# Optimization experiments

Hardware: AMD Instinct MI355X
Metric: run time of the kernel (lower is better)

Reference implementation:

```python
import jax, jax.numpy as jnp
import numpy as np

DIM = 4096
N_HEADS = 32
N_KV = 8
HEAD_DIM = DIM // N_HEADS  # 128
ROPE_THETA = 10000.0


def setup_inputs() -> dict:
    key = jax.random.key(0)
    ks = jax.random.split(key, 5)
    B, S = 1, 2048
    x = jax.random.normal(ks[0], (B, S, DIM), jnp.float32)
    wq = jax.random.normal(ks[1], (N_HEADS * HEAD_DIM, DIM), jnp.float32) * 0.02
    wk = jax.random.normal(ks[2], (N_KV * HEAD_DIM, DIM), jnp.float32) * 0.02
    wv = jax.random.normal(ks[3], (N_KV * HEAD_DIM, DIM), jnp.float32) * 0.02
    wo = jax.random.normal(ks[4], (DIM, DIM), jnp.float32) * 0.02
    # precomputed RoPE frequencies: angle[t, i] = t / theta^(2i/head_dim)
    inv_freq = 1.0 / (ROPE_THETA ** (jnp.arange(0, HEAD_DIM, 2, dtype=jnp.float32) / HEAD_DIM))
    t = jnp.arange(S, dtype=jnp.float32)
    angles = jnp.outer(t, inv_freq)  # [S, HEAD_DIM/2]
    return {"x": x, "wq": wq, "wk": wk, "wv": wv, "wo": wo,
            "freqs_cos": jnp.cos(angles), "freqs_sin": jnp.sin(angles)}


def _apply_rope(v, cos, sin):
    # v: [B, S, H, HEAD_DIM]; cos/sin: [S, HEAD_DIM/2]
    # mirrors torch view_as_complex on (..., hd/2, 2): even idx = real, odd idx = imag
    vr = v.reshape(*v.shape[:-1], HEAD_DIM // 2, 2)
    xr, xi = vr[..., 0], vr[..., 1]
    c = cos[None, :, None, :]
    s = sin[None, :, None, :]
    out_r = xr * c - xi * s
    out_i = xr * s + xi * c
    return jnp.stack([out_r, out_i], axis=-1).reshape(v.shape)


def reference(x, wq, wk, wv, wo, freqs_cos, freqs_sin):
    B, S, _ = x.shape
    rep = N_HEADS // N_KV
    q = (x @ wq.T).reshape(B, S, N_HEADS, HEAD_DIM)
    k = (x @ wk.T).reshape(B, S, N_KV, HEAD_DIM)
    v = (x @ wv.T).reshape(B, S, N_KV, HEAD_DIM)
    q = _apply_rope(q, freqs_cos, freqs_sin)
    k = _apply_rope(k, freqs_cos, freqs_sin)
    # native GQA: group query heads per kv head instead of materializing repeated KV
    qg = q.reshape(B, S, N_KV, rep, HEAD_DIM)
    scale = 1.0 / jnp.sqrt(jnp.asarray(HEAD_DIM, jnp.float32))
    scores = jnp.einsum('bqkrd,bskd->bkrqs', qg, k) * scale  # [B, n_kv, rep, S, S]
    causal = jnp.tril(jnp.ones((S, S), bool))
    scores = jnp.where(causal, scores, -jnp.inf)
    probs = jax.nn.softmax(scores, axis=-1)
    out = jnp.einsum('bkrqs,bskd->bqkrd', probs, v).reshape(B, S, DIM)
    return out @ wo.T
```

## Files before the change

kernel.cpp:

```cpp
#include <hip/hip_runtime.h>
#include <cstdint>

typedef __attribute__((ext_vector_type(8))) __bf16 bf16x8;
typedef __attribute__((ext_vector_type(4))) float  f32x4;
typedef __attribute__((ext_vector_type(8))) unsigned short ushort8;

#define DIM 4096
#define SEQ 2048
#define NH  32
#define NKV 8
#define HD  128

__device__ __forceinline__ float b2f(unsigned short u) {
  union { unsigned int i; float f; } v; v.i = ((unsigned int)u) << 16; return v.f;
}
__device__ __forceinline__ unsigned short f2b(float f) {
  union { float f; unsigned int i; } v; v.f = f;
  unsigned int r = v.i + 0x7fffu + ((v.i >> 16) & 1u);
  return (unsigned short)(r >> 16);
}

__device__ __forceinline__ void gl_lds16(const void* g, void* l) {
  __builtin_amdgcn_global_load_lds(
      (const __attribute__((address_space(1))) void*)(uintptr_t)g,
      (__attribute__((address_space(3))) void*)(uintptr_t)l,
      16, 0, 0);
}

__global__ __launch_bounds__(256) void f32_to_bf16(const float* __restrict__ src,
                                                   unsigned short* __restrict__ dst, int n) {
  const int i = (blockIdx.x * 256 + threadIdx.x) * 8;
  if (i >= n) return;
  const float4 a = *(const float4*)(src + i);
  const float4 b = *(const float4*)(src + i + 4);
  ushort8 o;
  o[0] = f2b(a.x); o[1] = f2b(a.y); o[2] = f2b(a.z); o[3] = f2b(a.w);
  o[4] = f2b(b.x); o[5] = f2b(b.y); o[6] = f2b(b.z); o[7] = f2b(b.w);
  *(ushort8*)(dst + i) = o;
}

template <bool OUT_F32>
__global__ __launch_bounds__(256) void gemm_bt(const unsigned short* __restrict__ A,
                                               const unsigned short* __restrict__ B,
                                               void* __restrict__ Cv,
                                               int M, int N, int K) {
  __shared__ __align__(16) unsigned short As[128 * 32];
  __shared__ __align__(16) unsigned short Bs[128 * 32];
  const int n0   = blockIdx.x * 128;
  const int m0   = blockIdx.y * 128;
  const int tid  = threadIdx.x;
  const int w    = tid >> 6;
  const int lane = tid & 63;
  const int quad = lane >> 4;
  const int l15  = lane & 15;
  const int wm   = (w & 1) * 64;
  const int wn   = (w >> 1) * 64;

  const f32x4 fzero = {0.f, 0.f, 0.f, 0.f};
  f32x4 acc[4][4];
#pragma unroll
  for (int i = 0; i < 4; ++i)
#pragma unroll
    for (int j = 0; j < 4; ++j) acc[i][j] = fzero;

  const int srow = lane >> 2;
  const int scol = (lane & 3) * 8;

  for (int k0 = 0; k0 < K; k0 += 32) {
    __syncthreads();
#pragma unroll
    for (int cc = 0; cc < 2; ++cc) {
      const int c   = w * 2 + cc;
      const int row = c * 16 + srow;
      gl_lds16(A + (size_t)(m0 + row) * K + k0 + scol, (char*)As + c * 1024);
      gl_lds16(B + (size_t)(n0 + row) * K + k0 + scol, (char*)Bs + c * 1024);
    }
    __syncthreads();

    bf16x8 af[4], bfr[4];
#pragma unroll
    for (int i = 0; i < 4; ++i) {
      af[i]  = *(const bf16x8*)(As + (wm + i * 16 + l15) * 32 + quad * 8);
      bfr[i] = *(const bf16x8*)(Bs + (wn + i * 16 + l15) * 32 + quad * 8);
    }
#pragma unroll
    for (int i = 0; i < 4; ++i)
#pragma unroll
      for (int j = 0; j < 4; ++j)
        acc[i][j] = __builtin_amdgcn_mfma_f32_16x16x32_bf16(af[i], bfr[j], acc[i][j], 0, 0, 0);
  }

#pragma unroll
  for (int i = 0; i < 4; ++i)
#pragma unroll
    for (int j = 0; j < 4; ++j) {
      const int m = m0 + wm + i * 16 + quad * 4;
      const int n = n0 + wn + j * 16 + l15;
      if (OUT_F32) {
        float* cp = (float*)Cv + (size_t)m * N + n;
#pragma unroll
        for (int r = 0; r < 4; ++r) cp[(size_t)r * N] = acc[i][j][r];
      } else {
        unsigned short* cp = (unsigned short*)Cv + (size_t)m * N + n;
#pragma unroll
        for (int r = 0; r < 4; ++r) cp[(size_t)r * N] = f2b(acc[i][j][r]);
      }
    }
}

template <bool OUT_F32>
__global__ __launch_bounds__(512, 2) void gemm256x192(const unsigned short* __restrict__ A,
                                                      const unsigned short* __restrict__ B,
                                                      void* __restrict__ Cv,
                                                      int M, int N, int K) {
  __shared__ __align__(16) unsigned short As[2][256 * 64];
  __shared__ __align__(16) unsigned short Bs[2][192 * 64];

  const int n0   = blockIdx.x * 192;
  const int m0   = blockIdx.y * 256;
  const int tid  = threadIdx.x;
  const int w    = tid >> 6;
  const int lane = tid & 63;
  const int quad = lane >> 4;
  const int l15  = lane & 15;
  const int wm   = (w >> 2) * 128;
  const int wn   = (w & 3) * 48;

  const int srow = lane >> 3;
  const int sgr  = (lane & 7) ^ srow;
  const unsigned short* aS = A + (size_t)(m0 + srow) * K + sgr * 8;
  const unsigned short* bS = B + (size_t)(n0 + srow) * K + sgr * 8;

  const int gr0 = ((quad)     ^ (l15 & 7)) * 8;
  const int gr1 = ((quad + 4) ^ (l15 & 7)) * 8;

  const f32x4 fzero = {0.f, 0.f, 0.f, 0.f};
  f32x4 acc[8][3];
#pragma unroll
  for (int i = 0; i < 8; ++i)
#pragma unroll
    for (int j = 0; j < 3; ++j) acc[i][j] = fzero;

  const int NT = K >> 6;

#pragma unroll
  for (int tp = 0; tp < 2; ++tp) {
#pragma unroll
    for (int i = 0; i < 4; ++i) {
      const int c = w * 4 + i;
      gl_lds16(aS + (size_t)c * 8 * K + tp * 64, (char*)As[tp] + c * 1024);
    }
#pragma unroll
    for (int i = 0; i < 3; ++i) {
      const int c = w * 3 + i;
      gl_lds16(bS + (size_t)c * 8 * K + tp * 64, (char*)Bs[tp] + c * 1024);
    }
  }

  for (int t = 0; t < NT; ++t) {
    const unsigned short* Ab = As[t & 1] + (wm + l15) * 64;
    const unsigned short* Bb = Bs[t & 1] + (wn + l15) * 64;

    if (t + 2 < NT) asm volatile("s_waitcnt vmcnt(7)" ::: "memory");
    else            asm volatile("s_waitcnt vmcnt(0)" ::: "memory");
    __builtin_amdgcn_s_barrier();
    __builtin_amdgcn_sched_barrier(0);

    bf16x8 af[8][2], bfr[3][2];
#pragma unroll
    for (int mf = 0; mf < 8; ++mf) {
      af[mf][0] = *(const bf16x8*)(Ab + mf * 1024 + gr0);
      af[mf][1] = *(const bf16x8*)(Ab + mf * 1024 + gr1);
    }
#pragma unroll
    for (int nf = 0; nf < 3; ++nf) {
      bfr[nf][0] = *(const bf16x8*)(Bb + nf * 1024 + gr0);
      bfr[nf][1] = *(const bf16x8*)(Bb + nf * 1024 + gr1);
    }

    __builtin_amdgcn_s_setprio(1);
#pragma unroll
    for (int ks = 0; ks < 2; ++ks)
#pragma unroll
      for (int mf = 0; mf < 4; ++mf)
#pragma unroll
        for (int nf = 0; nf < 3; ++nf)
          acc[mf][nf] = __builtin_amdgcn_mfma_f32_16x16x32_bf16(af[mf][ks], bfr[nf][ks],
                                                                acc[mf][nf], 0, 0, 0);
    __builtin_amdgcn_s_setprio(0);

    asm volatile("s_waitcnt lgkmcnt(0)" ::: "memory");
    __builtin_amdgcn_sched_barrier(0);
    __builtin_amdgcn_s_barrier();

    if (t + 2 < NT) {
      const int koff = (t + 2) * 64;
      unsigned short* Ad = As[t & 1];
      unsigned short* Bd = Bs[t & 1];
#pragma unroll
      for (int i = 0; i < 4; ++i) {
        const int c = w * 4 + i;
        gl_lds16(aS + (size_t)c * 8 * K + koff, (char*)Ad + c * 1024);
      }
#pragma unroll
      for (int i = 0; i < 3; ++i) {
        const int c = w * 3 + i;
        gl_lds16(bS + (size_t)c * 8 * K + koff, (char*)Bd + c * 1024);
      }
    }

    __builtin_amdgcn_s_setprio(1);
#pragma unroll
    for (int ks = 0; ks < 2; ++ks)
#pragma unroll
      for (int mf = 4; mf < 8; ++mf)
#pragma unroll
        for (int nf = 0; nf < 3; ++nf)
          acc[mf][nf] = __builtin_amdgcn_mfma_f32_16x16x32_bf16(af[mf][ks], bfr[nf][ks],
                                                                acc[mf][nf], 0, 0, 0);
    __builtin_amdgcn_s_setprio(0);
  }

#pragma unroll
  for (int mf = 0; mf < 8; ++mf)
#pragma unroll
    for (int nf = 0; nf < 3; ++nf) {
      const int m = m0 + wm + mf * 16 + quad * 4;
      const int n = n0 + wn + nf * 16 + l15;
      if (OUT_F32) {
        float* cp = (float*)Cv + (size_t)m * N + n;
#pragma unroll
        for (int r = 0; r < 4; ++r) cp[(size_t)r * N] = acc[mf][nf][r];
      } else {
        unsigned short* cp = (unsigned short*)Cv + (size_t)m * N + n;
#pragma unroll
        for (int r = 0; r < 4; ++r) cp[(size_t)r * N] = f2b(acc[mf][nf][r]);
      }
    }
}

template <bool OUT_F32>
__global__ __launch_bounds__(512, 2) void gemm128n256(const unsigned short* __restrict__ A,
                                                      const unsigned short* __restrict__ B,
                                                      void* __restrict__ Cv,
                                                      int M, int N, int K) {
  __shared__ __align__(16) unsigned short As[2][128 * 64];
  __shared__ __align__(16) unsigned short Bs[2][256 * 64];

  const int n0   = blockIdx.x * 256;
  const int m0   = blockIdx.y * 128;
  const int tid  = threadIdx.x;
  const int w    = tid >> 6;
  const int lane = tid & 63;
  const int quad = lane >> 4;
  const int l15  = lane & 15;
  const int wm   = (w >> 2) * 64;
  const int wn   = (w & 3) * 64;

  const int srow = lane >> 3;
  const int sgr  = (lane & 7) ^ srow;
  const unsigned short* aS = A + (size_t)(m0 + srow) * K + sgr * 8;
  const unsigned short* bS = B + (size_t)(n0 + srow) * K + sgr * 8;

  const int gr0 = ((quad)     ^ (l15 & 7)) * 8;
  const int gr1 = ((quad + 4) ^ (l15 & 7)) * 8;

  const f32x4 fzero = {0.f, 0.f, 0.f, 0.f};
  f32x4 acc[4][4];
#pragma unroll
  for (int i = 0; i < 4; ++i)
#pragma unroll
    for (int j = 0; j < 4; ++j) acc[i][j] = fzero;

  const int NT = K >> 6;

#pragma unroll
  for (int tp = 0; tp < 2; ++tp) {
#pragma unroll
    for (int i = 0; i < 2; ++i) {
      const int c = w * 2 + i;
      gl_lds16(aS + (size_t)c * 8 * K + tp * 64, (char*)As[tp] + c * 1024);
    }
#pragma unroll
    for (int i = 0; i < 4; ++i) {
      const int c = w * 4 + i;
      gl_lds16(bS + (size_t)c * 8 * K + tp * 64, (char*)Bs[tp] + c * 1024);
    }
  }

  for (int t = 0; t < NT; ++t) {
    const unsigned short* Ab = As[t & 1] + (wm + l15) * 64;
    const unsigned short* Bb = Bs[t & 1] + (wn + l15) * 64;

    if (t + 2 < NT) asm volatile("s_waitcnt vmcnt(6)" ::: "memory");
    else            asm volatile("s_waitcnt vmcnt(0)" ::: "memory");
    __builtin_amdgcn_s_barrier();
    __builtin_amdgcn_sched_barrier(0);

    bf16x8 af[4][2], bfr[4][2];
#pragma unroll
    for (int mf = 0; mf < 4; ++mf) {
      af[mf][0] = *(const bf16x8*)(Ab + mf * 1024 + gr0);
      af[mf][1] = *(const bf16x8*)(Ab + mf * 1024 + gr1);
    }
#pragma unroll
    for (int nf = 0; nf < 4; ++nf) {
      bfr[nf][0] = *(const bf16x8*)(Bb + nf * 1024 + gr0);
      bfr[nf][1] = *(const bf16x8*)(Bb + nf * 1024 + gr1);
    }

    __builtin_amdgcn_s_setprio(1);
#pragma unroll
    for (int ks = 0; ks < 2; ++ks)
#pragma unroll
      for (int mf = 0; mf < 2; ++mf)
#pragma unroll
        for (int nf = 0; nf < 4; ++nf)
          acc[mf][nf] = __builtin_amdgcn_mfma_f32_16x16x32_bf16(af[mf][ks], bfr[nf][ks],
                                                                acc[mf][nf], 0, 0, 0);
    __builtin_amdgcn_s_setprio(0);

    asm volatile("s_waitcnt lgkmcnt(0)" ::: "memory");
    __builtin_amdgcn_sched_barrier(0);
    __builtin_amdgcn_s_barrier();

    if (t + 2 < NT) {
      const int koff = (t + 2) * 64;
      unsigned short* Ad = As[t & 1];
      unsigned short* Bd = Bs[t & 1];
#pragma unroll
      for (int i = 0; i < 2; ++i) {
        const int c = w * 2 + i;
        gl_lds16(aS + (size_t)c * 8 * K + koff, (char*)Ad + c * 1024);
      }
#pragma unroll
      for (int i = 0; i < 4; ++i) {
        const int c = w * 4 + i;
        gl_lds16(bS + (size_t)c * 8 * K + koff, (char*)Bd + c * 1024);
      }
    }

    __builtin_amdgcn_s_setprio(1);
#pragma unroll
    for (int ks = 0; ks < 2; ++ks)
#pragma unroll
      for (int mf = 2; mf < 4; ++mf)
#pragma unroll
        for (int nf = 0; nf < 4; ++nf)
          acc[mf][nf] = __builtin_amdgcn_mfma_f32_16x16x32_bf16(af[mf][ks], bfr[nf][ks],
                                                                acc[mf][nf], 0, 0, 0);
    __builtin_amdgcn_s_setprio(0);
  }

#pragma unroll
  for (int mf = 0; mf < 4; ++mf)
#pragma unroll
    for (int nf = 0; nf < 4; ++nf) {
      const int m = m0 + wm + mf * 16 + quad * 4;
      const int n = n0 + wn + nf * 16 + l15;
      if (OUT_F32) {
        float* cp = (float*)Cv + (size_t)m * N + n;
#pragma unroll
        for (int r = 0; r < 4; ++r) cp[(size_t)r * N] = acc[mf][nf][r];
      } else {
        unsigned short* cp = (unsigned short*)Cv + (size_t)m * N + n;
#pragma unroll
        for (int r = 0; r < 4; ++r) cp[(size_t)r * N] = f2b(acc[mf][nf][r]);
      }
    }
}

__global__ void rope_kernel(unsigned short* __restrict__ q, int qstride,
                            unsigned short* __restrict__ k, int kstride,
                            const float* __restrict__ Ct, const float* __restrict__ St) {
  const int idx = blockIdx.x * 256 + threadIdx.x;
  const int total = SEQ * (NH * 64 + NKV * 64);
  if (idx >= total) return;
  const int s = idx / 2560;
  const int r = idx - s * 2560;
  unsigned short* base;
  int i;
  if (r < NH * 64) {
    const int h = r >> 6; i = r & 63;
    base = q + (size_t)s * qstride + h * HD + 2 * i;
  } else {
    const int r2 = r - NH * 64; const int h = r2 >> 6; i = r2 & 63;
    base = k + (size_t)s * kstride + h * HD + 2 * i;
  }
  const float c  = Ct[s * 64 + i];
  const float sn = St[s * 64 + i];
  const float xr = b2f(base[0]);
  const float xi = b2f(base[1]);
  base[0] = f2b(xr * c - xi * sn);
  base[1] = f2b(xr * sn + xi * c);
}

__global__ __launch_bounds__(256) void transpose_v(const unsigned short* __restrict__ v,
                                                   int vstride,
                                                   unsigned short* __restrict__ vt) {
  __shared__ unsigned short tile[64][72];
  const int bs = blockIdx.x;
  const int bd = blockIdx.y;
  const int t  = threadIdx.x;
  const int r  = t >> 2;
  const int c0 = (t & 3) * 16;
  const unsigned short* src = v + (size_t)(bs * 64 + r) * vstride + bd * 64 + c0;
#pragma unroll
  for (int i = 0; i < 2; ++i) {
    ushort8 d = *(const ushort8*)(src + i * 8);
#pragma unroll
    for (int e = 0; e < 8; ++e) tile[r][c0 + i * 8 + e] = d[e];
  }
  __syncthreads();
  unsigned short* dst = vt + (size_t)(bd * 64 + r) * SEQ + bs * 64 + c0;
#pragma unroll
  for (int i = 0; i < 2; ++i) {
    ushort8 o;
#pragma unroll
    for (int e = 0; e < 8; ++e) o[e] = tile[c0 + i * 8 + e][r];
    *(ushort8*)(dst + i * 8) = o;
  }
}

__global__ __launch_bounds__(256) void attn_kernel(const unsigned short* __restrict__ Q, int qstride,
                                                   const unsigned short* __restrict__ K, int kstride,
                                                   const unsigned short* __restrict__ VT,
                                                   unsigned short* __restrict__ O) {
  const int bid  = blockIdx.x;
  const int h    = bid & 31;
  const int pr   = bid >> 5;
  const int g    = h >> 2;
  const int tid  = threadIdx.x;
  const int w    = tid >> 6;
  const int lane = tid & 63;
  const int quad = lane >> 4;
  const int l15  = lane & 15;

  __shared__ __align__(16) unsigned short Ks[64 * 128];
  __shared__ __align__(16) unsigned short Vs[128 * 64];
  __shared__ __align__(16) unsigned short Ps[4][32 * 64];

  const float scale = 0.08838834764831845f;
  const f32x4 fzero = {0.f, 0.f, 0.f, 0.f};

  bf16x8 onesf;
#pragma unroll
  for (int e = 0; e < 8; ++e) onesf[e] = (__bf16)1.0f;

  const int ks_row = (lane >> 4);
  const int ks_q   = (lane & 15);
  const int vs_row = (lane >> 3);
  const int vs_q   = (lane & 7) ^ (lane >> 3);

  unsigned short* pw = Ps[w];

  for (int phase = 0; phase < 2; ++phase) {
    const int qt    = phase ? (15 - pr) : pr;
    const int qrow0 = qt * 128 + w * 32;

    bf16x8 qf[2][4];
#pragma unroll
    for (int gq = 0; gq < 2; ++gq) {
      const unsigned short* qb = Q + (size_t)(qrow0 + gq * 16 + l15) * qstride + h * HD + quad * 8;
#pragma unroll
      for (int c = 0; c < 4; ++c) qf[gq][c] = *(const bf16x8*)(qb + c * 32);
    }

    f32x4 oa[2][8];
    f32x4 ls[2];
#pragma unroll
    for (int gq = 0; gq < 2; ++gq) {
      ls[gq] = fzero;
#pragma unroll
      for (int i = 0; i < 8; ++i) oa[gq][i] = fzero;
    }

    const int n_tiles = 2 * qt + 2;

    for (int kt = 0; kt < n_tiles; ++kt) {
      const int kv0 = kt * 64;
      __syncthreads();
#pragma unroll
      for (int cc = 0; cc < 4; ++cc) {
        const int c = w * 4 + cc;
        {
          const int row = c * 4 + ks_row;
          const int qch = ks_q ^ (row & 15);
          gl_lds16(K + (size_t)(kv0 + row) * kstride + g * HD + qch * 8, (char*)Ks + c * 1024);
        }
        {
          const int row = c * 8 + vs_row;
          gl_lds16(VT + (size_t)(g * HD + row) * SEQ + kv0 + vs_q * 8, (char*)Vs + c * 1024);
        }
      }
      __syncthreads();

      f32x4 s[2][4];
#pragma unroll
      for (int gq = 0; gq < 2; ++gq)
#pragma unroll
        for (int ks = 0; ks < 4; ++ks) s[gq][ks] = fzero;
#pragma unroll
      for (int c = 0; c < 4; ++c)
#pragma unroll
        for (int ks = 0; ks < 4; ++ks) {
          const int row = ks * 16 + l15;
          const int p   = (c * 4 + quad) ^ l15;
          bf16x8 kf = *(const bf16x8*)(Ks + row * 128 + p * 8);
          s[0][ks] = __builtin_amdgcn_mfma_f32_16x16x32_bf16(qf[0][c], kf, s[0][ks], 0, 0, 0);
          s[1][ks] = __builtin_amdgcn_mfma_f32_16x16x32_bf16(qf[1][c], kf, s[1][ks], 0, 0, 0);
        }

#pragma unroll
      for (int gq = 0; gq < 2; ++gq)
#pragma unroll
        for (int r = 0; r < 4; ++r) {
          const int qrow = qrow0 + gq * 16 + quad * 4 + r;
          const int prow = gq * 16 + quad * 4 + r;
#pragma unroll
          for (int ks = 0; ks < 4; ++ks) {
            const float ex = __expf(s[gq][ks][r] * scale);
            const float e  = (kv0 + ks * 16 + l15 <= qrow) ? ex : 0.f;
            const int qc = ks * 2 + (l15 >> 3);
            const int p  = qc ^ (prow & 7);
            pw[prow * 64 + p * 8 + (l15 & 7)] = f2b(e);
          }
        }

#pragma unroll
      for (int ki = 0; ki < 2; ++ki) {
        bf16x8 pf[2];
#pragma unroll
        for (int gq = 0; gq < 2; ++gq) {
          const int row = gq * 16 + l15;
          const int p   = (ki * 4 + quad) ^ (l15 & 7);
          pf[gq] = *(const bf16x8*)(pw + row * 64 + p * 8);
        }
        ls[0] = __builtin_amdgcn_mfma_f32_16x16x32_bf16(pf[0], onesf, ls[0], 0, 0, 0);
        ls[1] = __builtin_amdgcn_mfma_f32_16x16x32_bf16(pf[1], onesf, ls[1], 0, 0, 0);
#pragma unroll
        for (int nt = 0; nt < 8; ++nt) {
          const int vrow = nt * 16 + l15;
          const int p    = (ki * 4 + quad) ^ (l15 & 7);
          bf16x8 vf = *(const bf16x8*)(Vs + vrow * 64 + p * 8);
          oa[0][nt] = __builtin_amdgcn_mfma_f32_16x16x32_bf16(pf[0], vf, oa[0][nt], 0, 0, 0);
          oa[1][nt] = __builtin_amdgcn_mfma_f32_16x16x32_bf16(pf[1], vf, oa[1][nt], 0, 0, 0);
        }
      }
    }

#pragma unroll
    for (int gq = 0; gq < 2; ++gq)
#pragma unroll
      for (int r = 0; r < 4; ++r) {
        const float inv = 1.f / ls[gq][r];
        const int qrow = qrow0 + gq * 16 + quad * 4 + r;
        unsigned short* orow = O + (size_t)qrow * DIM + h * HD;
#pragma unroll
        for (int nt = 0; nt < 8; ++nt) orow[nt * 16 + l15] = f2b(oa[gq][nt][r] * inv);
      }
  }
}

extern "C" void kernel_launch(void* const* d_in, const int* in_sizes, int n_in,
                              void* d_out, int out_size, void* d_ws, size_t ws_size,
                              hipStream_t stream) {
  const float* x  = (const float*)d_in[0];
  const float* wq = (const float*)d_in[1];
  const float* wk = (const float*)d_in[2];
  const float* wv = (const float*)d_in[3];
  const float* wo = (const float*)d_in[4];
  const float* fc = (const float*)d_in[5];
  const float* fs = (const float*)d_in[6];
  float* outp = (float*)d_out;

  const dim3 blk(256);
  const size_t M1 = 1024 * 1024;
  const int nx  = SEQ * DIM;
  const int nqw = DIM * DIM;
  const int nkw = NKV * HD * DIM;
  const int total = SEQ * (NH * 64 + NKV * 64);

  const size_t fused_elems = (8 + 24 + 12 + 2 + 8) * M1;

  if (ws_size >= fused_elems * 2) {
    unsigned short* xb   = (unsigned short*)d_ws;
    unsigned short* wbuf = xb   + 8  * M1;
    unsigned short* qkv  = wbuf + 24 * M1;
    unsigned short* vtb  = qkv  + 12 * M1;
    unsigned short* aob  = vtb  + 2  * M1;

    f32_to_bf16<<<dim3(nx  / 2048), blk, 0, stream>>>(x,  xb, nx);
    f32_to_bf16<<<dim3(nqw / 2048), blk, 0, stream>>>(wq, wbuf, nqw);
    f32_to_bf16<<<dim3(nkw / 2048), blk, 0, stream>>>(wk, wbuf + 16 * M1, nkw);
    f32_to_bf16<<<dim3(nkw / 2048), blk, 0, stream>>>(wv, wbuf + 20 * M1, nkw);

    gemm256x192<false><<<dim3(6144 / 192, SEQ / 256), dim3(512), 0, stream>>>(xb, wbuf, qkv,
                                                                              SEQ, 6144, DIM);

    rope_kernel<<<dim3((total + 255) / 256), blk, 0, stream>>>(qkv, 6144, qkv + 4096, 6144, fc, fs);
    transpose_v<<<dim3(SEQ / 64, 1024 / 64), blk, 0, stream>>>(qkv + 5120, 6144, vtb);
    attn_kernel<<<dim3(256), blk, 0, stream>>>(qkv, 6144, qkv + 4096, 6144, vtb, aob);

    f32_to_bf16<<<dim3(nqw / 2048), blk, 0, stream>>>(wo, wbuf, nqw);
    gemm128n256<true><<<dim3(DIM / 256, SEQ / 128), dim3(512), 0, stream>>>(aob, wbuf, outp,
                                                                            SEQ, DIM, DIM);
  } else {
    unsigned short* xb   = (unsigned short*)d_ws;
    unsigned short* wbuf = xb   + 8  * M1;
    unsigned short* qb   = wbuf + 16 * M1;
    unsigned short* kvb  = qb   + 8  * M1;
    unsigned short* vtb  = kvb  + 4  * M1;
    unsigned short* aob  = vtb  + 2  * M1;

    f32_to_bf16<<<dim3(nx  / 2048), blk, 0, stream>>>(x,  xb, nx);
    f32_to_bf16<<<dim3(nqw / 2048), blk, 0, stream>>>(wq, wbuf, nqw);
    gemm128n256<false><<<dim3(DIM / 256, SEQ / 128), dim3(512), 0, stream>>>(xb, wbuf, qb,
                                                                             SEQ, DIM, DIM);

    f32_to_bf16<<<dim3(nkw / 2048), blk, 0, stream>>>(wk, wbuf, nkw);
    f32_to_bf16<<<dim3(nkw / 2048), blk, 0, stream>>>(wv, wbuf + 4 * M1, nkw);
    gemm_bt<false><<<dim3(2048 / 128, SEQ / 128), blk, 0, stream>>>(xb, wbuf, kvb, SEQ, 2048, DIM);

    rope_kernel<<<dim3((total + 255) / 256), blk, 0, stream>>>(qb, 4096, kvb, 2048, fc, fs);
    transpose_v<<<dim3(SEQ / 64, 1024 / 64), blk, 0, stream>>>(kvb + 1024, 2048, vtb);
    attn_kernel<<<dim3(256), blk, 0, stream>>>(qb, 4096, kvb, 2048, vtb, aob);

    f32_to_bf16<<<dim3(nqw / 2048), blk, 0, stream>>>(wo, wbuf, nqw);
    gemm128n256<true><<<dim3(DIM / 256, SEQ / 128), dim3(512), 0, stream>>>(aob, wbuf, outp,
                                                                            SEQ, DIM, DIM);
  }
}
```

Baseline: 462.2 us.

## Restructure GEMM main loop to single-barrier, one-ahead prefetch with interleaved A fragment loads

Both bf16 GEMM kernels change from a two-tile-ahead prefetch with two barriers per K-step to a one-tile-ahead prefetch. Each iteration now does one full wait and one barrier, then issues the next tile's global-to-LDS loads into the other buffer. A fragments are read from LDS two at a time, interleaved with the MFMAs, instead of all being loaded up front, which lowers register pressure and per-iteration sync overhead. The cost is less global-load latency hiding, since each iteration waits for all outstanding loads (vmcnt(0)) before computing.

```diff
diff --git a/kernel.cpp b/kernel.cpp
--- a/kernel.cpp
+++ b/kernel.cpp
@@ -144,81 +144,65 @@
   const int NT = K >> 6;
 
 #pragma unroll
-  for (int tp = 0; tp < 2; ++tp) {
-#pragma unroll
-    for (int i = 0; i < 4; ++i) {
-      const int c = w * 4 + i;
-      gl_lds16(aS + (size_t)c * 8 * K + tp * 64, (char*)As[tp] + c * 1024);
-    }
-#pragma unroll
-    for (int i = 0; i < 3; ++i) {
-      const int c = w * 3 + i;
-      gl_lds16(bS + (size_t)c * 8 * K + tp * 64, (char*)Bs[tp] + c * 1024);
-    }
+  for (int i = 0; i < 4; ++i) {
+    const int c = w * 4 + i;
+    gl_lds16(aS + (size_t)c * 8 * K, (char*)As[0] + c * 1024);
+  }
+#pragma unroll
+  for (int i = 0; i < 3; ++i) {
+    const int c = w * 3 + i;
+    gl_lds16(bS + (size_t)c * 8 * K, (char*)Bs[0] + c * 1024);
   }
 
   for (int t = 0; t < NT; ++t) {
     const unsigned short* Ab = As[t & 1] + (wm + l15) * 64;
     const unsigned short* Bb = Bs[t & 1] + (wn + l15) * 64;
 
-    if (t + 2 < NT) asm volatile("s_waitcnt vmcnt(7)" ::: "memory");
-    else            asm volatile("s_waitcnt vmcnt(0)" ::: "memory");
+    asm volatile("s_waitcnt vmcnt(0) lgkmcnt(0)" ::: "memory");
     __builtin_amdgcn_s_barrier();
     __builtin_amdgcn_sched_barrier(0);
 
-    bf16x8 af[8][2], bfr[3][2];
-#pragma unroll
-    for (int mf = 0; mf < 8; ++mf) {
-      af[mf][0] = *(const bf16x8*)(Ab + mf * 1024 + gr0);
-      af[mf][1] = *(const bf16x8*)(Ab + mf * 1024 + gr1);
-    }
+    if (t + 1 < NT) {
+      const int koff = (t + 1) * 64;
+      unsigned short* Ad = As[(t + 1) & 1];
+      unsigned short* Bd = Bs[(t + 1) & 1];
+#pragma unroll
+      for (int i = 0; i < 4; ++i) {
+        const int c = w * 4 + i;
+        gl_lds16(aS + (size_t)c * 8 * K + koff, (char*)Ad + c * 1024);
+      }
+#pragma unroll
+      for (int i = 0; i < 3; ++i) {
+        const int c = w * 3 + i;
+        gl_lds16(bS + (size_t)c * 8 * K + koff, (char*)Bd + c * 1024);
+      }
+    }
+
+    bf16x8 bfr[3][2];
 #pragma unroll
     for (int nf = 0; nf < 3; ++nf) {
       bfr[nf][0] = *(const bf16x8*)(Bb + nf * 1024 + gr0);
       bfr[nf][1] = *(const bf16x8*)(Bb + nf * 1024 + gr1);
     }
-
-    __builtin_amdgcn_s_setprio(1);
-#pragma unroll
-    for (int ks = 0; ks < 2; ++ks)
-#pragma unroll
-      for (int mf = 0; mf < 4; ++mf)
-#pragma unroll
-        for (int nf = 0; nf < 3; ++nf)
-          acc[mf][nf] = __builtin_amdgcn_mfma_f32_16x16x32_bf16(af[mf][ks], bfr[nf][ks],
-                                                                acc[mf][nf], 0, 0, 0);
-    __builtin_amdgcn_s_setprio(0);
-
-    asm volatile("s_waitcnt lgkmcnt(0)" ::: "memory");
-    __builtin_amdgcn_sched_barrier(0);
-    __builtin_amdgcn_s_barrier();
-
-    if (t + 2 < NT) {
-      const int koff = (t + 2) * 64;
-      unsigned short* Ad = As[t & 1];
-      unsigned short* Bd = Bs[t & 1];
-#pragma unroll
-      for (int i = 0; i < 4; ++i) {
-        const int c = w * 4 + i;
-        gl_lds16(aS + (size_t)c * 8 * K + koff, (char*)Ad + c * 1024);
-      }
-#pragma unroll
-      for (int i = 0; i < 3; ++i) {
-        const int c = w * 3 + i;
-        gl_lds16(bS + (size_t)c * 8 * K + koff, (char*)Bd + c * 1024);
-      }
-    }
-
-    __builtin_amdgcn_s_setprio(1);
-#pragma unroll
-    for (int ks = 0; ks < 2; ++ks)
-#pragma unroll
-      for (int mf = 4; mf < 8; ++mf)
-#pragma unroll
-        for (int nf = 0; nf < 3; ++nf)
-          acc[mf][nf] = __builtin_amdgcn_mfma_f32_16x16x32_bf16(af[mf][ks], bfr[nf][ks],
-                                                                acc[mf][nf], 0, 0, 0);
-    __builtin_amdgcn_s_setprio(0);
+#pragma unroll
+    for (int mp = 0; mp < 4; ++mp) {
+      bf16x8 a0[2], a1[2];
+      a0[0] = *(const bf16x8*)(Ab + (mp * 2 + 0) * 1024 + gr0);
+      a0[1] = *(const bf16x8*)(Ab + (mp * 2 + 0) * 1024 + gr1);
+      a1[0] = *(const bf16x8*)(Ab + (mp * 2 + 1) * 1024 + gr0);
+      a1[1] = *(const bf16x8*)(Ab + (mp * 2 + 1) * 1024 + gr1);
+      __builtin_amdgcn_s_setprio(1);
+#pragma unroll
+      for (int ks = 0; ks < 2; ++ks)
+#pragma unroll
+        for (int nf = 0; nf < 3; ++nf) {
+          acc[mp * 2 + 0][nf] = __builtin_amdgcn_mfma_f32_16x16x32_bf16(a0[ks], bfr[nf][ks],
+                                                                        acc[mp * 2 + 0][nf], 0, 0, 0);
+          acc[mp * 2 + 1][nf] = __builtin_amdgcn_mfma_f32_16x16x32_bf16(a1[ks], bfr[nf][ks],
+                                                                        acc[mp * 2 + 1][nf], 0, 0, 0);
+        }
+      __builtin_amdgcn_s_setprio(0);
+    }
   }
 
 #pragma unroll
@@ -275,81 +259,65 @@
   const int NT = K >> 6;
 
 #pragma unroll
-  for (int tp = 0; tp < 2; ++tp) {
-#pragma unroll
-    for (int i = 0; i < 2; ++i) {
-      const int c = w * 2 + i;
-      gl_lds16(aS + (size_t)c * 8 * K + tp * 64, (char*)As[tp] + c * 1024);
-    }
-#pragma unroll
-    for (int i = 0; i < 4; ++i) {
-      const int c = w * 4 + i;
-      gl_lds16(bS + (size_t)c * 8 * K + tp * 64, (char*)Bs[tp] + c * 1024);
-    }
+  for (int i = 0; i < 2; ++i) {
+    const int c = w * 2 + i;
+    gl_lds16(aS + (size_t)c * 8 * K, (char*)As[0] + c * 1024);
+  }
+#pragma unroll
+  for (int i = 0; i < 4; ++i) {
+    const int c = w * 4 + i;
+    gl_lds16(bS + (size_t)c * 8 * K, (char*)Bs[0] + c * 1024);
   }
 
   for (int t = 0; t < NT; ++t) {
     const unsigned short* Ab = As[t & 1] + (wm + l15) * 64;
     const unsigned short* Bb = Bs[t & 1] + (wn + l15) * 64;
 
-    if (t + 2 < NT) asm volatile("s_waitcnt vmcnt(6)" ::: "memory");
-    else            asm volatile("s_waitcnt vmcnt(0)" ::: "memory");
+    asm volatile("s_waitcnt vmcnt(0) lgkmcnt(0)" ::: "memory");
     __builtin_amdgcn_s_barrier();
     __builtin_amdgcn_sched_barrier(0);
 
-    bf16x8 af[4][2], bfr[4][2];
-#pragma unroll
-    for (int mf = 0; mf < 4; ++mf) {
-      af[mf][0] = *(const bf16x8*)(Ab + mf * 1024 + gr0);
-      af[mf][1] = *(const bf16x8*)(Ab + mf * 1024 + gr1);
-    }
+    if (t + 1 < NT) {
+      const int koff = (t + 1) * 64;
+      unsigned short* Ad = As[(t + 1) & 1];
+      unsigned short* Bd = Bs[(t + 1) & 1];
+#pragma unroll
+      for (int i = 0; i < 2; ++i) {
+        const int c = w * 2 + i;
+        gl_lds16(aS + (size_t)c * 8 * K + koff, (char*)Ad + c * 1024);
+      }
+#pragma unroll
+      for (int i = 0; i < 4; ++i) {
+        const int c = w * 4 + i;
+        gl_lds16(bS + (size_t)c * 8 * K + koff, (char*)Bd + c * 1024);
+      }
+    }
+
+    bf16x8 bfr[4][2];
 #pragma unroll
     for (int nf = 0; nf < 4; ++nf) {
       bfr[nf][0] = *(const bf16x8*)(Bb + nf * 1024 + gr0);
       bfr[nf][1] = *(const bf16x8*)(Bb + nf * 1024 + gr1);
     }
-
-    __builtin_amdgcn_s_setprio(1);
-#pragma unroll
-    for (int ks = 0; ks < 2; ++ks)
-#pragma unroll
-      for (int mf = 0; mf < 2; ++mf)
-#pragma unroll
-        for (int nf = 0; nf < 4; ++nf)
-          acc[mf][nf] = __builtin_amdgcn_mfma_f32_16x16x32_bf16(af[mf][ks], bfr[nf][ks],
-                                                                acc[mf][nf], 0, 0, 0);
-    __builtin_amdgcn_s_setprio(0);
-
-    asm volatile("s_waitcnt lgkmcnt(0)" ::: "memory");
-    __builtin_amdgcn_sched_barrier(0);
-    __builtin_amdgcn_s_barrier();
-
-    if (t + 2 < NT) {
-      const int koff = (t + 2) * 64;
-      unsigned short* Ad = As[t & 1];
-      unsigned short* Bd = Bs[t & 1];
-#pragma unroll
-      for (int i = 0; i < 2; ++i) {
-        const int c = w * 2 + i;
-        gl_lds16(aS + (size_t)c * 8 * K + koff, (char*)Ad + c * 1024);
-      }
-#pragma unroll
-      for (int i = 0; i < 4; ++i) {
-        const int c = w * 4 + i;
-        gl_lds16(bS + (size_t)c * 8 * K + koff, (char*)Bd + c * 1024);
-      }
-    }
-
-    __builtin_amdgcn_s_setprio(1);
-#pragma unroll
-    for (int ks = 0; ks < 2; ++ks)
-#pragma unroll
-      for (int mf = 2; mf < 4; ++mf)
-#pragma unroll
-        for (int nf = 0; nf < 4; ++nf)
-          acc[mf][nf] = __builtin_amdgcn_mfma_f32_16x16x32_bf16(af[mf][ks], bfr[nf][ks],
-                                                                acc[mf][nf], 0, 0, 0);
-    __builtin_amdgcn_s_setprio(0);
+#pragma unroll
+    for (int mp = 0; mp < 2; ++mp) {
+      bf16x8 a0[2], a1[2];
+      a0[0] = *(const bf16x8*)(Ab + (mp * 2 + 0) * 1024 + gr0);
+      a0[1] = *(const bf16x8*)(Ab + (mp * 2 + 0) * 1024 + gr1);
+      a1[0] = *(const bf16x8*)(Ab + (mp * 2 + 1) * 1024 + gr0);
+      a1[1] = *(const bf16x8*)(Ab + (mp * 2 + 1) * 1024 + gr1);
+      __builtin_amdgcn_s_setprio(1);
+#pragma unroll
+      for (int ks = 0; ks < 2; ++ks)
+#pragma unroll
+        for (int nf = 0; nf < 4; ++nf) {
+          acc[mp * 2 + 0][nf] = __builtin_amdgcn_mfma_f32_16x16x32_bf16(a0[ks], bfr[nf][ks],
+                                                                        acc[mp * 2 + 0][nf], 0, 0, 0);
+          acc[mp * 2 + 1][nf] = __builtin_amdgcn_mfma_f32_16x16x32_bf16(a1[ks], bfr[nf][ks],
+                                                                        acc[mp * 2 + 1][nf], 0, 0, 0);
+        }
+      __builtin_amdgcn_s_setprio(0);
+    }
   }
 
 #pragma unroll
```

Result: no change. 460.8 us (-0.3%).
